# Optimization experiments

Measured on AMD Instinct MI355X. Metric: run time of the kernel, lower is better.

The kernel has to match this reference:

```python
import jax, jax.numpy as jnp
import numpy as np

BANDWIDTH = 0.1
N_STEPS = 5
TOL = 1e-3
BASE = 3
COORD_OFFSET = 512   # bins assumed within (-512, 511] per dim
COORD_BITS = 10      # 3 dims * 10 bits = 30 bits, fits int32


def _generate_offsets(d, base=3):
    # replicates torch.meshgrid(indexing='ij') over arange(-1, base-1)
    ranges = [np.arange(-1, base - 1) for _ in range(d)]
    mesh = np.meshgrid(*ranges, indexing='ij')
    return jnp.asarray(np.stack(mesh, axis=-1).reshape(-1, d), dtype=jnp.int32)


def _pack_keys(bins):
    # bins: (..., d) int32 -> unique scalar int32 key per bin coordinate
    d = bins.shape[-1]
    key = jnp.zeros(bins.shape[:-1], dtype=jnp.int32)
    for k in range(d):  # tiny fixed loop over dims
        key = (key << COORD_BITS) | (bins[..., k] + COORD_OFFSET)
    return key


def _step(X, offsets, bandwidth):
    # One mean-shift step: bin points, scatter-add sums/counts over the
    # union of offset-shifted bins (torch.unique replaced by exact key
    # packing + sort-based grouping, fixed shapes for jit).
    n, d = X.shape
    m = offsets.shape[0]  # base ** d
    bins = (X / bandwidth).astype(jnp.int32)          # trunc-toward-zero == torch .int()
    shifted = bins[:, None, :] + offsets[None, :, :]  # (n, m, d)
    keys = _pack_keys(shifted).reshape(-1)            # (n*m,)
    K = keys.shape[0]

    order = jnp.argsort(keys)
    skeys = keys[order]
    new_grp = jnp.concatenate(
        [jnp.zeros((1,), jnp.int32), (skeys[1:] != skeys[:-1]).astype(jnp.int32)]
    )
    seg = jnp.cumsum(new_grp)                         # group id per sorted position

    # X repeated once per offset (matches X.repeat(1, m).reshape(-1, d))
    Xflat = jnp.broadcast_to(X[:, None, :], (n, m, d)).reshape(-1, d)
    sum_per = jax.ops.segment_sum(Xflat[order], seg, num_segments=K)          # (K, d)
    cnt_per = jax.ops.segment_sum(jnp.ones((K,), X.dtype), seg, num_segments=K)

    # segment id per original (unsorted) flat position == inverse_indices
    seg_orig = jnp.zeros((K,), seg.dtype).at[order].set(seg)
    sum_mapped = sum_per[seg_orig].reshape(n, m, d).sum(axis=1)   # (n, d)
    cnt_mapped = cnt_per[seg_orig].reshape(n, m).sum(axis=1)      # (n,)
    return sum_mapped / cnt_mapped[:, None]


def setup_inputs() -> dict:
    key = jax.random.key(0)
    X = jax.random.normal(key, (200000, 3), dtype=jnp.float32)
    return {"X": X}


def reference(X):
    n, d = X.shape
    offsets = _generate_offsets(d, BASE)

    def body(carry, _):
        Xc, done = carry
        Xn = _step(Xc, offsets, BANDWIDTH)
        Xn = jnp.where(done, Xc, Xn)  # freeze once converged (== early break)
        conv = jnp.max(jnp.linalg.norm(Xn - Xc, axis=1)) <= TOL
        return (Xn, done | conv), None

    (Xout, _), _ = jax.lax.scan(body, (X, jnp.array(False)), None, length=N_STEPS)
    return Xout
```

## Files before the change

### kernel.cpp

```cpp
#include <hip/hip_runtime.h>


constexpr float BW   = 0.1f;
constexpr float TOL2 = 1e-6f;
constexpr int DIM  = 112, OFF = 56;
constexpr int DIM2 = DIM * DIM;
constexpr int CELLS = DIM * DIM * DIM;
constexpr int CLW = CELLS / 32;
constexpr int RDIM = 16, RC = 7;
constexpr int NREG = RDIM * RDIM * RDIM;
constexpr int RC3 = RC * RC * RC;
constexpr int NB_A = 128, BLK = 256;
constexpr int NF = 2048;
constexpr int IPB = 51;
constexpr float FPS = 16777216.0f;
constexpr double FPSI = 1.0 / 16777216.0;

typedef float vf2 __attribute__((ext_vector_type(2)));

__device__ __forceinline__ int clampb(int v) { return v < 0 ? 0 : (v > DIM - 1 ? DIM - 1 : v); }
__device__ __forceinline__ int binf(float v) { return clampb((int)(v / BW) + OFF); }
__device__ __forceinline__ int flatb(int bx, int by, int bz) { return (bx * DIM + by) * DIM + bz; }
__device__ __forceinline__ int regOf(int bx, int by, int bz) {
    return ((bx / RC) * RDIM + (by / RC)) * RDIM + (bz / RC);
}
__device__ __forceinline__ int lcOf(int bx, int by, int bz) {
    return ((bx % RC) * RC + (by % RC)) * RC + (bz % RC);
}

__device__ __forceinline__ void pk_add(float* p, float a, float b) {
#if defined(__has_builtin) && __has_builtin(__builtin_amdgcn_global_atomic_fadd_v2f32)
    vf2 v = {a, b};
    __builtin_amdgcn_global_atomic_fadd_v2f32((vf2*)p, v);
#else
    atomicAdd(p, a);
    atomicAdd(p + 1, b);
#endif
}

__launch_bounds__(BLK)
__global__ void k_histA(const float* __restrict__ X, int n, int* __restrict__ blockHist,
                        float4* __restrict__ zeroA, float4* __restrict__ zeroB) {
    __shared__ int h[NREG];
    for (int i = threadIdx.x; i < NREG; i += blockDim.x) h[i] = 0;
    __syncthreads();
    int stride = gridDim.x * blockDim.x;
    for (int i = blockIdx.x * blockDim.x + threadIdx.x; i < n; i += stride) {
        float x = X[3 * i + 0], y = X[3 * i + 1], z = X[3 * i + 2];
        atomicAdd(&h[regOf(binf(x), binf(y), binf(z))], 1);
    }
    __syncthreads();
    for (int i = threadIdx.x; i < NREG; i += blockDim.x)
        blockHist[blockIdx.x * NREG + i] = h[i];
    for (int i = blockIdx.x * blockDim.x + threadIdx.x; i < CELLS; i += stride) {
        zeroA[i] = make_float4(0.f, 0.f, 0.f, 0.f);
        zeroB[i] = make_float4(0.f, 0.f, 0.f, 0.f);
    }
}

__global__ void k_colscan(int* __restrict__ blockHist, int* __restrict__ regionPS) {
    int r = blockIdx.x * blockDim.x + threadIdx.x;
    if (r >= NREG) return;
    int run = 0;
    for (int b = 0; b < NB_A; ++b) {
        int idx = b * NREG + r;
        int v = blockHist[idx];
        blockHist[idx] = run;
        run += v;
    }
    regionPS[r] = run;
}

__launch_bounds__(1024)
__global__ void k_regprefix(int* __restrict__ regionPS) {
    __shared__ int buf[1024];
    int t = threadIdx.x;
    int v0 = regionPS[4 * t + 0], v1 = regionPS[4 * t + 1];
    int v2 = regionPS[4 * t + 2], v3 = regionPS[4 * t + 3];
    int s = v0 + v1 + v2 + v3;
    buf[t] = s;
    __syncthreads();
    for (int d = 1; d < 1024; d <<= 1) {
        int add = (t >= d) ? buf[t - d] : 0;
        __syncthreads();
        buf[t] += add;
        __syncthreads();
    }
    int excl = buf[t] - s;
    regionPS[4 * t + 0] = excl;
    regionPS[4 * t + 1] = excl + v0;
    regionPS[4 * t + 2] = excl + v0 + v1;
    regionPS[4 * t + 3] = excl + v0 + v1 + v2;
    if (t == 1023) regionPS[4096] = buf[1023];
}

__launch_bounds__(BLK)
__global__ void k_scatterA(const float* __restrict__ X, int n,
                           const int* __restrict__ blockHist,
                           const int* __restrict__ regionPS,
                           float4* __restrict__ bucket, float4* __restrict__ zeroC) {
    __shared__ int cur[NREG];
    for (int i = threadIdx.x; i < NREG; i += blockDim.x) cur[i] = 0;
    __syncthreads();
    int stride = gridDim.x * blockDim.x;
    for (int i = blockIdx.x * blockDim.x + threadIdx.x; i < n; i += stride) {
        float x = X[3 * i + 0], y = X[3 * i + 1], z = X[3 * i + 2];
        int r = regOf(binf(x), binf(y), binf(z));
        int pos = regionPS[r] + blockHist[blockIdx.x * NREG + r] + atomicAdd(&cur[r], 1);
        bucket[pos] = make_float4(x, y, z, __int_as_float(i));
    }
    for (int i = blockIdx.x * blockDim.x + threadIdx.x; i < CELLS; i += stride)
        zeroC[i] = make_float4(0.f, 0.f, 0.f, 0.f);
}

__launch_bounds__(BLK)
__global__ void k_binB(const float4* __restrict__ bucket, const int* __restrict__ regionPS,
                       float4* __restrict__ A, int* __restrict__ E0,
                       int* __restrict__ PIdx, int* __restrict__ gM0) {
    __shared__ unsigned long long aX[RC3], aY[RC3], aZ[RC3];
    __shared__ unsigned aC[RC3];
    __shared__ int cidx[RC3];
    __shared__ int cnt, cur, sBase;
    int r = blockIdx.x;
    for (int c = threadIdx.x; c < RC3; c += blockDim.x) {
        aX[c] = 0ull; aY[c] = 0ull; aZ[c] = 0ull; aC[c] = 0u;
    }
    if (threadIdx.x == 0) { cnt = 0; cur = 0; }
    __syncthreads();
    int start = regionPS[r], end = regionPS[r + 1];
    for (int i = start + threadIdx.x; i < end; i += blockDim.x) {
        float4 p = bucket[i];
        int lc = lcOf(binf(p.x), binf(p.y), binf(p.z));
        atomicAdd(&aX[lc], (unsigned long long)(long long)rintf(p.x * FPS));
        atomicAdd(&aY[lc], (unsigned long long)(long long)rintf(p.y * FPS));
        atomicAdd(&aZ[lc], (unsigned long long)(long long)rintf(p.z * FPS));
        atomicAdd(&aC[lc], 1u);
    }
    __syncthreads();
    int myc = 0;
    for (int c = threadIdx.x; c < RC3; c += blockDim.x)
        if (aC[c] > 0u) ++myc;
    if (myc) atomicAdd(&cnt, myc);
    __syncthreads();
    if (threadIdx.x == 0 && cnt > 0) sBase = atomicAdd(gM0, cnt);
    __syncthreads();
    int rx = r / (RDIM * RDIM), ry = (r / RDIM) % RDIM, rz = r % RDIM;
    for (int c = threadIdx.x; c < RC3; c += blockDim.x) {
        if (aC[c] > 0u) {
            int idx = sBase + atomicAdd(&cur, 1);
            cidx[c] = idx;
            int bx = rx * RC + c / (RC * RC);
            int by = ry * RC + (c / RC) % RC;
            int bz = rz * RC + c % RC;
            int b = flatb(bx, by, bz);
            E0[idx] = b;
            A[b] = make_float4((float)((double)(long long)aX[c] * FPSI),
                               (float)((double)(long long)aY[c] * FPSI),
                               (float)((double)(long long)aZ[c] * FPSI),
                               (float)aC[c]);
        }
    }
    __syncthreads();
    for (int i = start + threadIdx.x; i < end; i += blockDim.x) {
        float4 p = bucket[i];
        int lc = lcOf(binf(p.x), binf(p.y), binf(p.z));
        PIdx[__float_as_int(p.w)] = cidx[lc];
    }
}

__launch_bounds__(BLK)
__global__ void k_compactM(unsigned* __restrict__ mask, int* __restrict__ listOut,
                           int* __restrict__ pKout) {
    __shared__ int scan[BLK];
    __shared__ int sBase;
    int i = blockIdx.x * blockDim.x + threadIdx.x;
    unsigned w = (i < CLW) ? mask[i] : 0u;
    if (i < CLW && w) mask[i] = 0u;
    int c = __popc(w);
    scan[threadIdx.x] = c;
    __syncthreads();
    for (int d = 1; d < BLK; d <<= 1) {
        int add = (threadIdx.x >= (unsigned)d) ? scan[threadIdx.x - d] : 0;
        __syncthreads();
        scan[threadIdx.x] += add;
        __syncthreads();
    }
    if (threadIdx.x == BLK - 1) {
        int tot = scan[BLK - 1];
        sBase = tot ? atomicAdd(pKout, tot) : 0;
    }
    __syncthreads();
    int base = sBase + scan[threadIdx.x] - c;
    int bb = i * 32;
    while (w) {
        int b = __ffs(w) - 1;
        listOut[base++] = bb + b;
        w &= w - 1;
    }
}

__launch_bounds__(BLK)
__global__ void k_fused(
    const float4* __restrict__ src, const int* __restrict__ list, const int* __restrict__ pK,
    float4* __restrict__ REo, int* __restrict__ IDXo, float4* __restrict__ eposInit,
    float4* __restrict__ tgt, unsigned* __restrict__ clT,
    int updS, const float* __restrict__ X, int n, const int* __restrict__ PIdx,
    const float4* __restrict__ REp, const int* __restrict__ IDXp,
    const int* __restrict__ pM0, float4* __restrict__ epos,
    unsigned* __restrict__ notConv,
    const int* __restrict__ clearList, const int* __restrict__ pKc,
    float4* __restrict__ clearGrid, int lastStep) {
    __shared__ float4 sh[BLK];
    __shared__ unsigned sFlag;
    if (threadIdx.x == 0) sFlag = 0;
    __syncthreads();
    int K = *pK;
    int NC = (K + IPB - 1) / IPB;
    int BC = NC;
    if (BC > NF - 256) BC = NF - 256;
    const float t5[5] = {1.f, 2.f, 3.f, 2.f, 1.f};
    bool moved = false;

    if ((int)blockIdx.x < BC) {
        int first, last, step;
        if (BC >= 64) {
            int xcd = blockIdx.x & 7, loc = blockIdx.x >> 3;
            int cpx = (NC + 7) >> 3;
            int bpx = ((BC - 1 - xcd) >> 3) + 1;
            first = xcd * cpx + loc;
            last = (xcd + 1) * cpx; if (last > NC) last = NC;
            step = bpx;
        } else {
            first = blockIdx.x; last = NC; step = BC;
        }
        for (int ib = first; ib < last; ib += step) {
            int li = threadIdx.x / 5;
            int dx = threadIdx.x % 5;
            int item = ib * IPB + li;
            float4 part = make_float4(0.f, 0.f, 0.f, 0.f);
            if (li < IPB && item < K) {
                int b = list[item];
                int bx = b / DIM2, rem = b % DIM2;
                int by = rem / DIM, bz = rem % DIM;
                int ix = bx + dx - 2;
                if ((unsigned)ix < (unsigned)DIM) {
                    float wx = t5[dx];
                    if (by >= 2 && by <= DIM - 3 && bz >= 2 && bz <= DIM - 3) {
                        #pragma unroll
                        for (int dy = 0; dy < 5; ++dy) {
                            float wxy = wx * t5[dy];
                            const float4* row = src + flatb(ix, by + dy - 2, bz - 2);
                            #pragma unroll
                            for (int dz = 0; dz < 5; ++dz) {
                                float w = wxy * t5[dz];
                                float4 e = row[dz];
                                part.x = fmaf(w, e.x, part.x);
                                part.y = fmaf(w, e.y, part.y);
                                part.z = fmaf(w, e.z, part.z);
                                part.w = fmaf(w, e.w, part.w);
                            }
                        }
                    } else {
                        for (int dy = 0; dy < 5; ++dy) {
                            int iy = by + dy - 2;
                            if ((unsigned)iy >= (unsigned)DIM) continue;
                            float wxy = wx * t5[dy];
                            for (int dz = 0; dz < 5; ++dz) {
                                int iz = bz + dz - 2;
                                if ((unsigned)iz >= (unsigned)DIM) continue;
                                float w = wxy * t5[dz];
                                float4 e = src[flatb(ix, iy, iz)];
                                part.x = fmaf(w, e.x, part.x);
                                part.y = fmaf(w, e.y, part.y);
                                part.z = fmaf(w, e.z, part.z);
                                part.w = fmaf(w, e.w, part.w);
                            }
                        }
                    }
                }
            }
            sh[threadIdx.x] = part;
            __syncthreads();
            if (threadIdx.x < 64) {
                int item2 = ib * IPB + threadIdx.x;
                bool valid = (threadIdx.x < IPB) && (item2 < K);
                int bn = -1;
                float4 sv = make_float4(0.f, 0.f, 0.f, 0.f);
                if (valid) {
                    int base5 = threadIdx.x * 5;
                    float4 a0 = sh[base5 + 0], a1 = sh[base5 + 1], a2 = sh[base5 + 2];
                    float4 a3 = sh[base5 + 3], a4 = sh[base5 + 4];
                    float sx = a0.x + a1.x + a2.x + a3.x + a4.x;
                    float sy = a0.y + a1.y + a2.y + a3.y + a4.y;
                    float sz = a0.z + a1.z + a2.z + a3.z + a4.z;
                    float sc = a0.w + a1.w + a2.w + a3.w + a4.w;
                    int b = list[item2];
                    float W = src[b].w;
                    float4 np = make_float4(sx / sc, sy / sc, sz / sc, W);
                    REo[item2] = np;
                    IDXo[b] = item2;
                    if (eposInit) eposInit[item2] = np;
                    if (!lastStep) {
                        bn = flatb(binf(np.x), binf(np.y), binf(np.z));
                        sv = make_float4(W * np.x, W * np.y, W * np.z, W);
                    }
                }
                if (!lastStep) {
                    int pbn = __shfl_up(bn, 1, 64);
                    unsigned f = (threadIdx.x == 0 || pbn != bn) ? 1u : 0u;
                    unsigned nf = __shfl_down(f, 1, 64);
                    bool leader = valid && (threadIdx.x == 63 || nf != 0u);
                    #pragma unroll
                    for (int off = 1; off < 64; off <<= 1) {
                        float ox = __shfl_up(sv.x, off, 64);
                        float oy = __shfl_up(sv.y, off, 64);
                        float oz = __shfl_up(sv.z, off, 64);
                        float ow = __shfl_up(sv.w, off, 64);
                        unsigned of = __shfl_up(f, off, 64);
                        if ((int)threadIdx.x >= off) {
                            if (!f) { sv.x += ox; sv.y += oy; sv.z += oz; sv.w += ow; }
                            f |= of;
                        }
                    }
                    if (leader) {
                        float* cell = (float*)&tgt[bn];
                        pk_add(cell + 0, sv.x, sv.y);
                        pk_add(cell + 2, sv.z, sv.w);
                        atomicOr(&clT[(unsigned)bn >> 5], 1u << (bn & 31));
                    }
                }
            }
            __syncthreads();
        }
    } else {
        int U = (updS > 0) ? (X ? n : *pM0) : 0;
        int CL = clearList ? *pKc : 0;
        int total = U + CL;
        bool done = false;
        if (updS > 1) {
            for (int t = 1; t < updS; ++t) done |= (notConv[t] == 0u);
        }
        int stride = (NF - BC) * blockDim.x;
        for (int idx = (blockIdx.x - BC) * blockDim.x + threadIdx.x; idx < total;
             idx += stride) {
            if (idx < U) {
                int e = idx;
                if (X) {
                    float x = X[3 * e + 0], y = X[3 * e + 1], z = X[3 * e + 2];
                    float4 rr = REp[PIdx[e]];
                    float ex = rr.x - x, ey = rr.y - y, ez = rr.z - z;
                    moved |= (fmaf(ex, ex, fmaf(ey, ey, ez * ez)) > TOL2);
                } else if (!done) {
                    float4 p = epos[e];
                    int j = IDXp[flatb(binf(p.x), binf(p.y), binf(p.z))];
                    float4 rr = REp[j];
                    float ex = rr.x - p.x, ey = rr.y - p.y, ez = rr.z - p.z;
                    moved |= (fmaf(ex, ex, fmaf(ey, ey, ez * ez)) > TOL2);
                    epos[e] = make_float4(rr.x, rr.y, rr.z, p.w);
                }
            } else {
                clearGrid[clearList[idx - U]] = make_float4(0.f, 0.f, 0.f, 0.f);
            }
        }
    }
    if (moved) sFlag = 1;
    __syncthreads();
    if (threadIdx.x == 0 && updS > 0 && sFlag) notConv[updS] = 1u;
}

__launch_bounds__(BLK)
__global__ void k_fin(const float4* __restrict__ REa, const int* __restrict__ IDXa,
                      const float4* __restrict__ epos, const int* __restrict__ pM0,
                      const unsigned* __restrict__ notConv, float4* __restrict__ fpos) {
    int M0 = *pM0;
    bool done = false;
    for (int t = 1; t <= 4; ++t) done |= (notConv[t] == 0u);
    for (int e = blockIdx.x * blockDim.x + threadIdx.x; e < M0;
         e += gridDim.x * blockDim.x) {
        float4 p = epos[e];
        if (!done) {
            float4 rr = REa[IDXa[flatb(binf(p.x), binf(p.y), binf(p.z))]];
            p.x = rr.x; p.y = rr.y; p.z = rr.z;
        }
        fpos[e] = p;
    }
}

__global__ void k_map(const int* __restrict__ PIdx, int n, const float4* __restrict__ fpos,
                      float* __restrict__ out) {
    int i = blockIdx.x * blockDim.x + threadIdx.x;
    if (i >= n) return;
    float4 p = fpos[PIdx[i]];
    out[3 * i + 0] = p.x;
    out[3 * i + 1] = p.y;
    out[3 * i + 2] = p.z;
}

extern "C" void kernel_launch(void* const* d_in, const int* in_sizes, int n_in,
                              void* d_out, int out_size, void* d_ws, size_t ws_size,
                              hipStream_t stream) {
    const float* X = (const float*)d_in[0];
    int n = in_sizes[0] / 3;

    char* ws = (char*)d_ws;
    int*      cnt     = (int*)ws;
    unsigned* notConv = (unsigned*)(ws + 32);
    size_t mB = (size_t)CLW * 4;
    size_t gB = (size_t)CELLS * 16;
    unsigned* m0 = (unsigned*)(ws + 256);
    unsigned* m1 = (unsigned*)(ws + 256 + mB);
    float4* A = (float4*)(ws + 256 + 2 * mB);
    float4* B = (float4*)((char*)A + gB);
    float4* C = (float4*)((char*)B + gB);
    int* IDXa = (int*)((char*)C + gB);
    int* IDXb = IDXa + CELLS;
    float4* REa  = (float4*)(IDXb + CELLS);
    float4* REb  = REa + n;
    float4* epos = REb + n;
    int* E0   = (int*)(epos + n);
    int* La   = E0 + n;
    int* Lb   = La + n;
    int* Lc   = Lb + n;
    int* Ld   = Lc + n;
    int* PIdx = Ld + n;
    float4* bucket = (float4*)(PIdx + n);
    int* blockHist = (int*)(bucket + n);
    int* regionPS  = blockHist + NB_A * NREG;

    hipMemsetAsync(ws, 0, 256 + 2 * mB, stream);

    const int NCM = (CLW + BLK - 1) / BLK;

    k_histA<<<NB_A, BLK, 0, stream>>>(X, n, blockHist, A, B);
    k_colscan<<<NREG / BLK, BLK, 0, stream>>>(blockHist, regionPS);
    k_regprefix<<<1, 1024, 0, stream>>>(regionPS);
    k_scatterA<<<NB_A, BLK, 0, stream>>>(X, n, blockHist, regionPS, bucket, C);
    k_binB<<<NREG, BLK, 0, stream>>>(bucket, regionPS, A, E0, PIdx, &cnt[1]);

    k_fused<<<NF, BLK, 0, stream>>>(A, E0, &cnt[1], REa, IDXa, epos,
                                    B, m0,
                                    0, nullptr, n, nullptr, nullptr, nullptr, nullptr,
                                    nullptr, notConv, nullptr, nullptr, nullptr, 0);
    k_compactM<<<NCM, BLK, 0, stream>>>(m0, La, &cnt[2]);
    k_fused<<<NF, BLK, 0, stream>>>(B, La, &cnt[2], REb, IDXb, nullptr,
                                    C, m1,
                                    1, X, n, PIdx, REa, IDXa, &cnt[1], nullptr,
                                    notConv, E0, &cnt[1], A, 0);
    k_compactM<<<NCM, BLK, 0, stream>>>(m1, Lb, &cnt[3]);
    k_fused<<<NF, BLK, 0, stream>>>(C, Lb, &cnt[3], REa, IDXa, nullptr,
                                    A, m0,
                                    2, nullptr, n, nullptr, REb, IDXb, &cnt[1], epos,
                                    notConv, La, &cnt[2], B, 0);
    k_compactM<<<NCM, BLK, 0, stream>>>(m0, Lc, &cnt[4]);
    k_fused<<<NF, BLK, 0, stream>>>(A, Lc, &cnt[4], REb, IDXb, nullptr,
                                    B, m1,
                                    3, nullptr, n, nullptr, REa, IDXa, &cnt[1], epos,
                                    notConv, nullptr, nullptr, nullptr, 0);
    k_compactM<<<NCM, BLK, 0, stream>>>(m1, Ld, &cnt[5]);
    k_fused<<<NF, BLK, 0, stream>>>(B, Ld, &cnt[5], REa, IDXa, nullptr,
                                    nullptr, nullptr,
                                    4, nullptr, n, nullptr, REb, IDXb, &cnt[1], epos,
                                    notConv, nullptr, nullptr, nullptr, 1);

    k_fin<<<256, BLK, 0, stream>>>(REa, IDXa, epos, &cnt[1], notConv, REb);
    k_map<<<(n + BLK - 1) / BLK, BLK, 0, stream>>>(PIdx, n, REb, (float*)d_out);
}
```

Measured before the change: 246.5 us.

## Build occupied-cell lists inside fused step via atomicOr; fold final lookup into map

The separate bitmask-compaction kernel that ran after each step is removed. The fused kernel now uses the old value returned by atomicOr to detect cells it newly marks, and appends them to the next occupied-cell list with a wave ballot plus one atomicAdd per wavefront. Mask words are cleared later by the update blocks, which walk the previous list. The final-position kernel is merged into the output map kernel, which removes two launches and one intermediate buffer pass. In exchange, list order becomes nondeterministic, cells are no longer sorted, and the per-wave global atomic adds contention.

Measured after the change: 290.1 us. 1.18x slower.

```diff
diff --git a/kernel.cpp b/kernel.cpp
--- a/kernel.cpp
+++ b/kernel.cpp
@@ -169,47 +169,19 @@
 }
 
 __launch_bounds__(BLK)
-__global__ void k_compactM(unsigned* __restrict__ mask, int* __restrict__ listOut,
-                           int* __restrict__ pKout) {
-    __shared__ int scan[BLK];
-    __shared__ int sBase;
-    int i = blockIdx.x * blockDim.x + threadIdx.x;
-    unsigned w = (i < CLW) ? mask[i] : 0u;
-    if (i < CLW && w) mask[i] = 0u;
-    int c = __popc(w);
-    scan[threadIdx.x] = c;
-    __syncthreads();
-    for (int d = 1; d < BLK; d <<= 1) {
-        int add = (threadIdx.x >= (unsigned)d) ? scan[threadIdx.x - d] : 0;
-        __syncthreads();
-        scan[threadIdx.x] += add;
-        __syncthreads();
-    }
-    if (threadIdx.x == BLK - 1) {
-        int tot = scan[BLK - 1];
-        sBase = tot ? atomicAdd(pKout, tot) : 0;
-    }
-    __syncthreads();
-    int base = sBase + scan[threadIdx.x] - c;
-    int bb = i * 32;
-    while (w) {
-        int b = __ffs(w) - 1;
-        listOut[base++] = bb + b;
-        w &= w - 1;
-    }
-}
-
-__launch_bounds__(BLK)
 __global__ void k_fused(
     const float4* __restrict__ src, const int* __restrict__ list, const int* __restrict__ pK,
     float4* __restrict__ REo, int* __restrict__ IDXo, float4* __restrict__ eposInit,
     float4* __restrict__ tgt, unsigned* __restrict__ clT,
+    int* __restrict__ listOut, int* __restrict__ pKout,
     int updS, const float* __restrict__ X, int n, const int* __restrict__ PIdx,
     const float4* __restrict__ REp, const int* __restrict__ IDXp,
     const int* __restrict__ pM0, float4* __restrict__ epos,
     unsigned* __restrict__ notConv,
     const int* __restrict__ clearList, const int* __restrict__ pKc,
-    float4* __restrict__ clearGrid, int lastStep) {
+    float4* __restrict__ clearGrid,
+    const int* __restrict__ mClrList, const int* __restrict__ pKm,
+    unsigned* __restrict__ mClr, int lastStep) {
     __shared__ float4 sh[BLK];
     __shared__ unsigned sFlag;
     if (threadIdx.x == 0) sFlag = 0;
@@ -322,11 +294,22 @@
                             f |= of;
                         }
                     }
+                    bool fset = false;
                     if (leader) {
                         float* cell = (float*)&tgt[bn];
                         pk_add(cell + 0, sv.x, sv.y);
                         pk_add(cell + 2, sv.z, sv.w);
-                        atomicOr(&clT[(unsigned)bn >> 5], 1u << (bn & 31));
+                        unsigned bit = 1u << (bn & 31);
+                        unsigned old = atomicOr(&clT[(unsigned)bn >> 5], bit);
+                        fset = (old & bit) == 0u;
+                    }
+                    unsigned long long bal = __ballot(fset);
+                    if (bal) {
+                        int base = 0;
+                        if (threadIdx.x == 0) base = atomicAdd(pKout, __popcll(bal));
+                        base = __shfl(base, 0, 64);
+                        if (fset)
+                            listOut[base + __popcll(bal & ((1ull << threadIdx.x) - 1ull))] = bn;
                     }
                 }
             }
@@ -335,7 +318,8 @@
     } else {
         int U = (updS > 0) ? (X ? n : *pM0) : 0;
         int CL = clearList ? *pKc : 0;
-        int total = U + CL;
+        int CM = mClrList ? *pKm : 0;
+        int total = U + CL + CM;
         bool done = false;
         if (updS > 1) {
             for (int t = 1; t < updS; ++t) done |= (notConv[t] == 0u);
@@ -358,8 +342,11 @@
                     moved |= (fmaf(ex, ex, fmaf(ey, ey, ez * ez)) > TOL2);
                     epos[e] = make_float4(rr.x, rr.y, rr.z, p.w);
                 }
+            } else if (idx < U + CL) {
+                clearGrid[clearList[idx - U]] = make_float4(0.f, 0.f, 0.f, 0.f);
             } else {
-                clearGrid[clearList[idx - U]] = make_float4(0.f, 0.f, 0.f, 0.f);
+                int b = mClrList[idx - U - CL];
+                mClr[(unsigned)b >> 5] = 0u;
             }
         }
     }
@@ -368,29 +355,18 @@
     if (threadIdx.x == 0 && updS > 0 && sFlag) notConv[updS] = 1u;
 }
 
-__launch_bounds__(BLK)
-__global__ void k_fin(const float4* __restrict__ REa, const int* __restrict__ IDXa,
-                      const float4* __restrict__ epos, const int* __restrict__ pM0,
-                      const unsigned* __restrict__ notConv, float4* __restrict__ fpos) {
-    int M0 = *pM0;
+__global__ void k_map(const int* __restrict__ PIdx, int n, const float4* __restrict__ epos,
+                      const float4* __restrict__ REa, const int* __restrict__ IDXa,
+                      const unsigned* __restrict__ notConv, float* __restrict__ out) {
     bool done = false;
     for (int t = 1; t <= 4; ++t) done |= (notConv[t] == 0u);
-    for (int e = blockIdx.x * blockDim.x + threadIdx.x; e < M0;
-         e += gridDim.x * blockDim.x) {
-        float4 p = epos[e];
-        if (!done) {
-            float4 rr = REa[IDXa[flatb(binf(p.x), binf(p.y), binf(p.z))]];
-            p.x = rr.x; p.y = rr.y; p.z = rr.z;
-        }
-        fpos[e] = p;
-    }
-}
-
-__global__ void k_map(const int* __restrict__ PIdx, int n, const float4* __restrict__ fpos,
-                      float* __restrict__ out) {
     int i = blockIdx.x * blockDim.x + threadIdx.x;
     if (i >= n) return;
-    float4 p = fpos[PIdx[i]];
+    float4 p = epos[PIdx[i]];
+    if (!done) {
+        float4 rr = REa[IDXa[flatb(binf(p.x), binf(p.y), binf(p.z))]];
+        p.x = rr.x; p.y = rr.y; p.z = rr.z;
+    }
     out[3 * i + 0] = p.x;
     out[3 * i + 1] = p.y;
     out[3 * i + 2] = p.z;
@@ -429,8 +405,6 @@
 
     hipMemsetAsync(ws, 0, 256 + 2 * mB, stream);
 
-    const int NCM = (CLW + BLK - 1) / BLK;
-
     k_histA<<<NB_A, BLK, 0, stream>>>(X, n, blockHist, A, B);
     k_colscan<<<NREG / BLK, BLK, 0, stream>>>(blockHist, regionPS);
     k_regprefix<<<1, 1024, 0, stream>>>(regionPS);
@@ -438,30 +412,36 @@
     k_binB<<<NREG, BLK, 0, stream>>>(bucket, regionPS, A, E0, PIdx, &cnt[1]);
 
     k_fused<<<NF, BLK, 0, stream>>>(A, E0, &cnt[1], REa, IDXa, epos,
-                                    B, m0,
+                                    B, m0, La, &cnt[2],
                                     0, nullptr, n, nullptr, nullptr, nullptr, nullptr,
-                                    nullptr, notConv, nullptr, nullptr, nullptr, 0);
-    k_compactM<<<NCM, BLK, 0, stream>>>(m0, La, &cnt[2]);
+                                    nullptr, notConv,
+                                    nullptr, nullptr, nullptr,
+                                    nullptr, nullptr, nullptr, 0);
     k_fused<<<NF, BLK, 0, stream>>>(B, La, &cnt[2], REb, IDXb, nullptr,
-                                    C, m1,
+                                    C, m1, Lb, &cnt[3],
                                     1, X, n, PIdx, REa, IDXa, &cnt[1], nullptr,
-                                    notConv, E0, &cnt[1], A, 0);
-    k_compactM<<<NCM, BLK, 0, stream>>>(m1, Lb, &cnt[3]);
+                                    notConv,
+                                    E0, &cnt[1], A,
+                                    La, &cnt[2], m0, 0);
     k_fused<<<NF, BLK, 0, stream>>>(C, Lb, &cnt[3], REa, IDXa, nullptr,
-                                    A, m0,
+                                    A, m0, Lc, &cnt[4],
                                     2, nullptr, n, nullptr, REb, IDXb, &cnt[1], epos,
-                                    notConv, La, &cnt[2], B, 0);
-    k_compactM<<<NCM, BLK, 0, stream>>>(m0, Lc, &cnt[4]);
+                                    notConv,
+                                    La, &cnt[2], B,
+                                    Lb, &cnt[3], m1, 0);
     k_fused<<<NF, BLK, 0, stream>>>(A, Lc, &cnt[4], REb, IDXb, nullptr,
-                                    B, m1,
+                                    B, m1, Ld, &cnt[5],
                                     3, nullptr, n, nullptr, REa, IDXa, &cnt[1], epos,
-                                    notConv, nullptr, nullptr, nullptr, 0);
-    k_compactM<<<NCM, BLK, 0, stream>>>(m1, Ld, &cnt[5]);
+                                    notConv,
+                                    nullptr, nullptr, nullptr,
+                                    nullptr, nullptr, nullptr, 0);
     k_fused<<<NF, BLK, 0, stream>>>(B, Ld, &cnt[5], REa, IDXa, nullptr,
-                                    nullptr, nullptr,
+                                    nullptr, nullptr, nullptr, nullptr,
                                     4, nullptr, n, nullptr, REb, IDXb, &cnt[1], epos,
-                                    notConv, nullptr, nullptr, nullptr, 1);
-
-    k_fin<<<256, BLK, 0, stream>>>(REa, IDXa, epos, &cnt[1], notConv, REb);
-    k_map<<<(n + BLK - 1) / BLK, BLK, 0, stream>>>(PIdx, n, REb, (float*)d_out);
-}
+                                    notConv,
+                                    nullptr, nullptr, nullptr,
+                                    nullptr, nullptr, nullptr, 1);
+
+    k_map<<<(n + BLK - 1) / BLK, BLK, 0, stream>>>(PIdx, n, epos, REa, IDXa,
+                                                   notConv, (float*)d_out);
+}
```

## Split separable 5x5x5 stencil into dense z-pass and sparse xy-pass

Applied to the files above, without the earlier changes.

Replaces the per-cell 125-tap stencil with a separable scheme. A dense pass convolves the whole grid along z into a temporary buffer. A sparse pass then does only the 25 x/y taps per active cell, reading the z-presummed values. This cuts gathers per active cell from 125 to 25, but adds a full-grid read and write every step plus an extra kernel launch. It also reduces ping-pong grids from three to two, drops the separate grid zeroing and k_fin, and folds the final position lookup into k_map.

New measurement: 282.0 us. 14.4% more time.

```diff
diff --git a/kernel.cpp b/kernel.cpp
--- a/kernel.cpp
+++ b/kernel.cpp
@@ -13,6 +13,8 @@
 constexpr int NB_A = 128, BLK = 256;
 constexpr int NF = 2048;
 constexpr int IPB = 51;
+constexpr int NZ4 = CELLS / 4;
+constexpr int BCZ = NF - 256;
 constexpr float FPS = 16777216.0f;
 constexpr double FPSI = 1.0 / 16777216.0;
 
@@ -98,7 +100,7 @@
 __global__ void k_scatterA(const float* __restrict__ X, int n,
                            const int* __restrict__ blockHist,
                            const int* __restrict__ regionPS,
-                           float4* __restrict__ bucket, float4* __restrict__ zeroC) {
+                           float4* __restrict__ bucket) {
     __shared__ int cur[NREG];
     for (int i = threadIdx.x; i < NREG; i += blockDim.x) cur[i] = 0;
     __syncthreads();
@@ -109,8 +111,6 @@
         int pos = regionPS[r] + blockHist[blockIdx.x * NREG + r] + atomicAdd(&cur[r], 1);
         bucket[pos] = make_float4(x, y, z, __int_as_float(i));
     }
-    for (int i = blockIdx.x * blockDim.x + threadIdx.x; i < CELLS; i += stride)
-        zeroC[i] = make_float4(0.f, 0.f, 0.f, 0.f);
 }
 
 __launch_bounds__(BLK)
@@ -169,168 +169,38 @@
 }
 
 __launch_bounds__(BLK)
-__global__ void k_compactM(unsigned* __restrict__ mask, int* __restrict__ listOut,
-                           int* __restrict__ pKout) {
-    __shared__ int scan[BLK];
-    __shared__ int sBase;
-    int i = blockIdx.x * blockDim.x + threadIdx.x;
-    unsigned w = (i < CLW) ? mask[i] : 0u;
-    if (i < CLW && w) mask[i] = 0u;
-    int c = __popc(w);
-    scan[threadIdx.x] = c;
-    __syncthreads();
-    for (int d = 1; d < BLK; d <<= 1) {
-        int add = (threadIdx.x >= (unsigned)d) ? scan[threadIdx.x - d] : 0;
-        __syncthreads();
-        scan[threadIdx.x] += add;
-        __syncthreads();
-    }
-    if (threadIdx.x == BLK - 1) {
-        int tot = scan[BLK - 1];
-        sBase = tot ? atomicAdd(pKout, tot) : 0;
-    }
-    __syncthreads();
-    int base = sBase + scan[threadIdx.x] - c;
-    int bb = i * 32;
-    while (w) {
-        int b = __ffs(w) - 1;
-        listOut[base++] = bb + b;
-        w &= w - 1;
-    }
-}
-
-__launch_bounds__(BLK)
-__global__ void k_fused(
-    const float4* __restrict__ src, const int* __restrict__ list, const int* __restrict__ pK,
-    float4* __restrict__ REo, int* __restrict__ IDXo, float4* __restrict__ eposInit,
-    float4* __restrict__ tgt, unsigned* __restrict__ clT,
-    int updS, const float* __restrict__ X, int n, const int* __restrict__ PIdx,
-    const float4* __restrict__ REp, const int* __restrict__ IDXp,
-    const int* __restrict__ pM0, float4* __restrict__ epos,
-    unsigned* __restrict__ notConv,
-    const int* __restrict__ clearList, const int* __restrict__ pKc,
-    float4* __restrict__ clearGrid, int lastStep) {
-    __shared__ float4 sh[BLK];
+__global__ void k_zconv(const float4* __restrict__ src, float4* __restrict__ T1,
+                        int updS, const float* __restrict__ X, int n,
+                        const int* __restrict__ PIdx,
+                        const float4* __restrict__ REp, const int* __restrict__ IDXp,
+                        const int* __restrict__ pM0, float4* __restrict__ epos,
+                        unsigned* __restrict__ notConv,
+                        const int* __restrict__ clearList, const int* __restrict__ pKc,
+                        float4* __restrict__ clearGrid) {
     __shared__ unsigned sFlag;
     if (threadIdx.x == 0) sFlag = 0;
     __syncthreads();
-    int K = *pK;
-    int NC = (K + IPB - 1) / IPB;
-    int BC = NC;
-    if (BC > NF - 256) BC = NF - 256;
-    const float t5[5] = {1.f, 2.f, 3.f, 2.f, 1.f};
     bool moved = false;
-
-    if ((int)blockIdx.x < BC) {
-        int first, last, step;
-        if (BC >= 64) {
-            int xcd = blockIdx.x & 7, loc = blockIdx.x >> 3;
-            int cpx = (NC + 7) >> 3;
-            int bpx = ((BC - 1 - xcd) >> 3) + 1;
-            first = xcd * cpx + loc;
-            last = (xcd + 1) * cpx; if (last > NC) last = NC;
-            step = bpx;
-        } else {
-            first = blockIdx.x; last = NC; step = BC;
-        }
-        for (int ib = first; ib < last; ib += step) {
-            int li = threadIdx.x / 5;
-            int dx = threadIdx.x % 5;
-            int item = ib * IPB + li;
-            float4 part = make_float4(0.f, 0.f, 0.f, 0.f);
-            if (li < IPB && item < K) {
-                int b = list[item];
-                int bx = b / DIM2, rem = b % DIM2;
-                int by = rem / DIM, bz = rem % DIM;
-                int ix = bx + dx - 2;
-                if ((unsigned)ix < (unsigned)DIM) {
-                    float wx = t5[dx];
-                    if (by >= 2 && by <= DIM - 3 && bz >= 2 && bz <= DIM - 3) {
-                        #pragma unroll
-                        for (int dy = 0; dy < 5; ++dy) {
-                            float wxy = wx * t5[dy];
-                            const float4* row = src + flatb(ix, by + dy - 2, bz - 2);
-                            #pragma unroll
-                            for (int dz = 0; dz < 5; ++dz) {
-                                float w = wxy * t5[dz];
-                                float4 e = row[dz];
-                                part.x = fmaf(w, e.x, part.x);
-                                part.y = fmaf(w, e.y, part.y);
-                                part.z = fmaf(w, e.z, part.z);
-                                part.w = fmaf(w, e.w, part.w);
-                            }
-                        }
-                    } else {
-                        for (int dy = 0; dy < 5; ++dy) {
-                            int iy = by + dy - 2;
-                            if ((unsigned)iy >= (unsigned)DIM) continue;
-                            float wxy = wx * t5[dy];
-                            for (int dz = 0; dz < 5; ++dz) {
-                                int iz = bz + dz - 2;
-                                if ((unsigned)iz >= (unsigned)DIM) continue;
-                                float w = wxy * t5[dz];
-                                float4 e = src[flatb(ix, iy, iz)];
-                                part.x = fmaf(w, e.x, part.x);
-                                part.y = fmaf(w, e.y, part.y);
-                                part.z = fmaf(w, e.z, part.z);
-                                part.w = fmaf(w, e.w, part.w);
-                            }
-                        }
-                    }
-                }
-            }
-            sh[threadIdx.x] = part;
-            __syncthreads();
-            if (threadIdx.x < 64) {
-                int item2 = ib * IPB + threadIdx.x;
-                bool valid = (threadIdx.x < IPB) && (item2 < K);
-                int bn = -1;
-                float4 sv = make_float4(0.f, 0.f, 0.f, 0.f);
-                if (valid) {
-                    int base5 = threadIdx.x * 5;
-                    float4 a0 = sh[base5 + 0], a1 = sh[base5 + 1], a2 = sh[base5 + 2];
-                    float4 a3 = sh[base5 + 3], a4 = sh[base5 + 4];
-                    float sx = a0.x + a1.x + a2.x + a3.x + a4.x;
-                    float sy = a0.y + a1.y + a2.y + a3.y + a4.y;
-                    float sz = a0.z + a1.z + a2.z + a3.z + a4.z;
-                    float sc = a0.w + a1.w + a2.w + a3.w + a4.w;
-                    int b = list[item2];
-                    float W = src[b].w;
-                    float4 np = make_float4(sx / sc, sy / sc, sz / sc, W);
-                    REo[item2] = np;
-                    IDXo[b] = item2;
-                    if (eposInit) eposInit[item2] = np;
-                    if (!lastStep) {
-                        bn = flatb(binf(np.x), binf(np.y), binf(np.z));
-                        sv = make_float4(W * np.x, W * np.y, W * np.z, W);
-                    }
-                }
-                if (!lastStep) {
-                    int pbn = __shfl_up(bn, 1, 64);
-                    unsigned f = (threadIdx.x == 0 || pbn != bn) ? 1u : 0u;
-                    unsigned nf = __shfl_down(f, 1, 64);
-                    bool leader = valid && (threadIdx.x == 63 || nf != 0u);
-                    #pragma unroll
-                    for (int off = 1; off < 64; off <<= 1) {
-                        float ox = __shfl_up(sv.x, off, 64);
-                        float oy = __shfl_up(sv.y, off, 64);
-                        float oz = __shfl_up(sv.z, off, 64);
-                        float ow = __shfl_up(sv.w, off, 64);
-                        unsigned of = __shfl_up(f, off, 64);
-                        if ((int)threadIdx.x >= off) {
-                            if (!f) { sv.x += ox; sv.y += oy; sv.z += oz; sv.w += ow; }
-                            f |= of;
-                        }
-                    }
-                    if (leader) {
-                        float* cell = (float*)&tgt[bn];
-                        pk_add(cell + 0, sv.x, sv.y);
-                        pk_add(cell + 2, sv.z, sv.w);
-                        atomicOr(&clT[(unsigned)bn >> 5], 1u << (bn & 31));
-                    }
-                }
-            }
-            __syncthreads();
+    if ((int)blockIdx.x < BCZ) {
+        for (int w = blockIdx.x * BLK + threadIdx.x; w < NZ4; w += BCZ * BLK) {
+            int c0 = w * 4;
+            int z0 = c0 % DIM;
+            float4 e[8];
+            #pragma unroll
+            for (int k = 0; k < 8; ++k) {
+                int z = z0 + k - 2;
+                if ((unsigned)z < (unsigned)DIM) e[k] = src[c0 + k - 2];
+                else e[k] = make_float4(0.f, 0.f, 0.f, 0.f);
+            }
+            #pragma unroll
+            for (int j = 0; j < 4; ++j) {
+                float4 r;
+                r.x = e[j].x + e[j + 4].x + 2.f * (e[j + 1].x + e[j + 3].x) + 3.f * e[j + 2].x;
+                r.y = e[j].y + e[j + 4].y + 2.f * (e[j + 1].y + e[j + 3].y) + 3.f * e[j + 2].y;
+                r.z = e[j].z + e[j + 4].z + 2.f * (e[j + 1].z + e[j + 3].z) + 3.f * e[j + 2].z;
+                r.w = e[j].w + e[j + 4].w + 2.f * (e[j + 1].w + e[j + 3].w) + 3.f * e[j + 2].w;
+                T1[c0 + j] = r;
+            }
         }
     } else {
         int U = (updS > 0) ? (X ? n : *pM0) : 0;
@@ -340,8 +210,8 @@
         if (updS > 1) {
             for (int t = 1; t < updS; ++t) done |= (notConv[t] == 0u);
         }
-        int stride = (NF - BC) * blockDim.x;
-        for (int idx = (blockIdx.x - BC) * blockDim.x + threadIdx.x; idx < total;
+        int stride = (NF - BCZ) * BLK;
+        for (int idx = (blockIdx.x - BCZ) * BLK + threadIdx.x; idx < total;
              idx += stride) {
             if (idx < U) {
                 int e = idx;
@@ -369,28 +239,165 @@
 }
 
 __launch_bounds__(BLK)
-__global__ void k_fin(const float4* __restrict__ REa, const int* __restrict__ IDXa,
-                      const float4* __restrict__ epos, const int* __restrict__ pM0,
-                      const unsigned* __restrict__ notConv, float4* __restrict__ fpos) {
-    int M0 = *pM0;
+__global__ void k_conv(const float4* __restrict__ T1, const float4* __restrict__ src,
+                       const int* __restrict__ list, const int* __restrict__ pK,
+                       float4* __restrict__ REo, int* __restrict__ IDXo,
+                       float4* __restrict__ eposInit,
+                       float4* __restrict__ tgt, unsigned* __restrict__ clT,
+                       int lastStep) {
+    __shared__ float4 sh[BLK];
+    int K = *pK;
+    int NC = (K + IPB - 1) / IPB;
+    int BC = NC > NF ? NF : NC;
+    if ((int)blockIdx.x >= BC) return;
+    const float t5[5] = {1.f, 2.f, 3.f, 2.f, 1.f};
+
+    int first, last, step;
+    if (BC >= 64) {
+        int xcd = blockIdx.x & 7, loc = blockIdx.x >> 3;
+        int cpx = (NC + 7) >> 3;
+        int bpx = ((BC - 1 - xcd) >> 3) + 1;
+        first = xcd * cpx + loc;
+        last = (xcd + 1) * cpx; if (last > NC) last = NC;
+        step = bpx;
+    } else {
+        first = blockIdx.x; last = NC; step = BC;
+    }
+    for (int ib = first; ib < last; ib += step) {
+        int li = threadIdx.x / 5;
+        int dx = threadIdx.x % 5;
+        int item = ib * IPB + li;
+        float4 part = make_float4(0.f, 0.f, 0.f, 0.f);
+        if (li < IPB && item < K) {
+            int b = list[item];
+            int bx = b / DIM2, rem = b % DIM2;
+            int by = rem / DIM, bz = rem % DIM;
+            int ix = bx + dx - 2;
+            if ((unsigned)ix < (unsigned)DIM) {
+                float wx = t5[dx];
+                if (by >= 2 && by <= DIM - 3) {
+                    const float4* col = T1 + flatb(ix, by - 2, bz);
+                    #pragma unroll
+                    for (int dy = 0; dy < 5; ++dy) {
+                        float w = wx * t5[dy];
+                        float4 e = col[dy * DIM];
+                        part.x = fmaf(w, e.x, part.x);
+                        part.y = fmaf(w, e.y, part.y);
+                        part.z = fmaf(w, e.z, part.z);
+                        part.w = fmaf(w, e.w, part.w);
+                    }
+                } else {
+                    for (int dy = 0; dy < 5; ++dy) {
+                        int iy = by + dy - 2;
+                        if ((unsigned)iy >= (unsigned)DIM) continue;
+                        float w = wx * t5[dy];
+                        float4 e = T1[flatb(ix, iy, bz)];
+                        part.x = fmaf(w, e.x, part.x);
+                        part.y = fmaf(w, e.y, part.y);
+                        part.z = fmaf(w, e.z, part.z);
+                        part.w = fmaf(w, e.w, part.w);
+                    }
+                }
+            }
+        }
+        sh[threadIdx.x] = part;
+        __syncthreads();
+        if (threadIdx.x < 64) {
+            int item2 = ib * IPB + threadIdx.x;
+            bool valid = (threadIdx.x < IPB) && (item2 < K);
+            int bn = -1;
+            float4 sv = make_float4(0.f, 0.f, 0.f, 0.f);
+            if (valid) {
+                int base5 = threadIdx.x * 5;
+                float4 a0 = sh[base5 + 0], a1 = sh[base5 + 1], a2 = sh[base5 + 2];
+                float4 a3 = sh[base5 + 3], a4 = sh[base5 + 4];
+                float sx = a0.x + a1.x + a2.x + a3.x + a4.x;
+                float sy = a0.y + a1.y + a2.y + a3.y + a4.y;
+                float sz = a0.z + a1.z + a2.z + a3.z + a4.z;
+                float sc = a0.w + a1.w + a2.w + a3.w + a4.w;
+                int b = list[item2];
+                float W = src[b].w;
+                float4 np = make_float4(sx / sc, sy / sc, sz / sc, W);
+                REo[item2] = np;
+                IDXo[b] = item2;
+                if (eposInit) eposInit[item2] = np;
+                if (!lastStep) {
+                    bn = flatb(binf(np.x), binf(np.y), binf(np.z));
+                    sv = make_float4(W * np.x, W * np.y, W * np.z, W);
+                }
+            }
+            if (!lastStep) {
+                int pbn = __shfl_up(bn, 1, 64);
+                unsigned f = (threadIdx.x == 0 || pbn != bn) ? 1u : 0u;
+                unsigned nf = __shfl_down(f, 1, 64);
+                bool leader = valid && (threadIdx.x == 63 || nf != 0u);
+                #pragma unroll
+                for (int off = 1; off < 64; off <<= 1) {
+                    float ox = __shfl_up(sv.x, off, 64);
+                    float oy = __shfl_up(sv.y, off, 64);
+                    float oz = __shfl_up(sv.z, off, 64);
+                    float ow = __shfl_up(sv.w, off, 64);
+                    unsigned of = __shfl_up(f, off, 64);
+                    if ((int)threadIdx.x >= off) {
+                        if (!f) { sv.x += ox; sv.y += oy; sv.z += oz; sv.w += ow; }
+                        f |= of;
+                    }
+                }
+                if (leader) {
+                    float* cell = (float*)&tgt[bn];
+                    pk_add(cell + 0, sv.x, sv.y);
+                    pk_add(cell + 2, sv.z, sv.w);
+                    atomicOr(&clT[(unsigned)bn >> 5], 1u << (bn & 31));
+                }
+            }
+        }
+        __syncthreads();
+    }
+}
+
+__launch_bounds__(BLK)
+__global__ void k_compactM(unsigned* __restrict__ mask, int* __restrict__ listOut,
+                           int* __restrict__ pKout) {
+    __shared__ int scan[BLK];
+    __shared__ int sBase;
+    int i = blockIdx.x * blockDim.x + threadIdx.x;
+    unsigned w = (i < CLW) ? mask[i] : 0u;
+    if (i < CLW && w) mask[i] = 0u;
+    int c = __popc(w);
+    scan[threadIdx.x] = c;
+    __syncthreads();
+    for (int d = 1; d < BLK; d <<= 1) {
+        int add = (threadIdx.x >= (unsigned)d) ? scan[threadIdx.x - d] : 0;
+        __syncthreads();
+        scan[threadIdx.x] += add;
+        __syncthreads();
+    }
+    if (threadIdx.x == BLK - 1) {
+        int tot = scan[BLK - 1];
+        sBase = tot ? atomicAdd(pKout, tot) : 0;
+    }
+    __syncthreads();
+    int base = sBase + scan[threadIdx.x] - c;
+    int bb = i * 32;
+    while (w) {
+        int b = __ffs(w) - 1;
+        listOut[base++] = bb + b;
+        w &= w - 1;
+    }
+}
+
+__global__ void k_map(const int* __restrict__ PIdx, int n, const float4* __restrict__ epos,
+                      const float4* __restrict__ REa, const int* __restrict__ IDXa,
+                      const unsigned* __restrict__ notConv, float* __restrict__ out) {
     bool done = false;
     for (int t = 1; t <= 4; ++t) done |= (notConv[t] == 0u);
-    for (int e = blockIdx.x * blockDim.x + threadIdx.x; e < M0;
-         e += gridDim.x * blockDim.x) {
-        float4 p = epos[e];
-        if (!done) {
-            float4 rr = REa[IDXa[flatb(binf(p.x), binf(p.y), binf(p.z))]];
-            p.x = rr.x; p.y = rr.y; p.z = rr.z;
-        }
-        fpos[e] = p;
-    }
-}
-
-__global__ void k_map(const int* __restrict__ PIdx, int n, const float4* __restrict__ fpos,
-                      float* __restrict__ out) {
     int i = blockIdx.x * blockDim.x + threadIdx.x;
     if (i >= n) return;
-    float4 p = fpos[PIdx[i]];
+    float4 p = epos[PIdx[i]];
+    if (!done) {
+        float4 rr = REa[IDXa[flatb(binf(p.x), binf(p.y), binf(p.z))]];
+        p.x = rr.x; p.y = rr.y; p.z = rr.z;
+    }
     out[3 * i + 0] = p.x;
     out[3 * i + 1] = p.y;
     out[3 * i + 2] = p.z;
@@ -409,10 +416,10 @@
     size_t gB = (size_t)CELLS * 16;
     unsigned* m0 = (unsigned*)(ws + 256);
     unsigned* m1 = (unsigned*)(ws + 256 + mB);
-    float4* A = (float4*)(ws + 256 + 2 * mB);
-    float4* B = (float4*)((char*)A + gB);
-    float4* C = (float4*)((char*)B + gB);
-    int* IDXa = (int*)((char*)C + gB);
+    float4* A  = (float4*)(ws + 256 + 2 * mB);
+    float4* B  = (float4*)((char*)A + gB);
+    float4* T1 = (float4*)((char*)B + gB);
+    int* IDXa = (int*)((char*)T1 + gB);
     int* IDXb = IDXa + CELLS;
     float4* REa  = (float4*)(IDXb + CELLS);
     float4* REb  = REa + n;
@@ -434,34 +441,34 @@
     k_histA<<<NB_A, BLK, 0, stream>>>(X, n, blockHist, A, B);
     k_colscan<<<NREG / BLK, BLK, 0, stream>>>(blockHist, regionPS);
     k_regprefix<<<1, 1024, 0, stream>>>(regionPS);
-    k_scatterA<<<NB_A, BLK, 0, stream>>>(X, n, blockHist, regionPS, bucket, C);
+    k_scatterA<<<NB_A, BLK, 0, stream>>>(X, n, blockHist, regionPS, bucket);
     k_binB<<<NREG, BLK, 0, stream>>>(bucket, regionPS, A, E0, PIdx, &cnt[1]);
 
-    k_fused<<<NF, BLK, 0, stream>>>(A, E0, &cnt[1], REa, IDXa, epos,
-                                    B, m0,
-                                    0, nullptr, n, nullptr, nullptr, nullptr, nullptr,
-                                    nullptr, notConv, nullptr, nullptr, nullptr, 0);
+    k_zconv<<<NF, BLK, 0, stream>>>(A, T1, 0, nullptr, n, nullptr, nullptr, nullptr,
+                                    nullptr, nullptr, notConv, nullptr, nullptr, nullptr);
+    k_conv<<<NF, BLK, 0, stream>>>(T1, A, E0, &cnt[1], REa, IDXa, epos, B, m0, 0);
     k_compactM<<<NCM, BLK, 0, stream>>>(m0, La, &cnt[2]);
-    k_fused<<<NF, BLK, 0, stream>>>(B, La, &cnt[2], REb, IDXb, nullptr,
-                                    C, m1,
-                                    1, X, n, PIdx, REa, IDXa, &cnt[1], nullptr,
-                                    notConv, E0, &cnt[1], A, 0);
+
+    k_zconv<<<NF, BLK, 0, stream>>>(B, T1, 1, X, n, PIdx, REa, IDXa, &cnt[1],
+                                    nullptr, notConv, E0, &cnt[1], A);
+    k_conv<<<NF, BLK, 0, stream>>>(T1, B, La, &cnt[2], REb, IDXb, nullptr, A, m1, 0);
     k_compactM<<<NCM, BLK, 0, stream>>>(m1, Lb, &cnt[3]);
-    k_fused<<<NF, BLK, 0, stream>>>(C, Lb, &cnt[3], REa, IDXa, nullptr,
-                                    A, m0,
-                                    2, nullptr, n, nullptr, REb, IDXb, &cnt[1], epos,
-                                    notConv, La, &cnt[2], B, 0);
+
+    k_zconv<<<NF, BLK, 0, stream>>>(A, T1, 2, nullptr, n, nullptr, REb, IDXb, &cnt[1],
+                                    epos, notConv, La, &cnt[2], B);
+    k_conv<<<NF, BLK, 0, stream>>>(T1, A, Lb, &cnt[3], REa, IDXa, nullptr, B, m0, 0);
     k_compactM<<<NCM, BLK, 0, stream>>>(m0, Lc, &cnt[4]);
-    k_fused<<<NF, BLK, 0, stream>>>(A, Lc, &cnt[4], REb, IDXb, nullptr,
-                                    B, m1,
-                                    3, nullptr, n, nullptr, REa, IDXa, &cnt[1], epos,
-                                    notConv, nullptr, nullptr, nullptr, 0);
+
+    k_zconv<<<NF, BLK, 0, stream>>>(B, T1, 3, nullptr, n, nullptr, REa, IDXa, &cnt[1],
+                                    epos, notConv, Lb, &cnt[3], A);
+    k_conv<<<NF, BLK, 0, stream>>>(T1, B, Lc, &cnt[4], REb, IDXb, nullptr, A, m1, 0);
     k_compactM<<<NCM, BLK, 0, stream>>>(m1, Ld, &cnt[5]);
-    k_fused<<<NF, BLK, 0, stream>>>(B, Ld, &cnt[5], REa, IDXa, nullptr,
-                                    nullptr, nullptr,
-                                    4, nullptr, n, nullptr, REb, IDXb, &cnt[1], epos,
-                                    notConv, nullptr, nullptr, nullptr, 1);
-
-    k_fin<<<256, BLK, 0, stream>>>(REa, IDXa, epos, &cnt[1], notConv, REb);
-    k_map<<<(n + BLK - 1) / BLK, BLK, 0, stream>>>(PIdx, n, REb, (float*)d_out);
-}
+
+    k_zconv<<<NF, BLK, 0, stream>>>(A, T1, 4, nullptr, n, nullptr, REb, IDXb, &cnt[1],
+                                    epos, notConv, nullptr, nullptr, nullptr);
+    k_conv<<<NF, BLK, 0, stream>>>(T1, A, Ld, &cnt[5], REa, IDXa, nullptr,
+                                   nullptr, nullptr, 1);
+
+    k_map<<<(n + BLK - 1) / BLK, BLK, 0, stream>>>(PIdx, n, epos, REa, IDXa,
+                                                   notConv, (float*)d_out);
+}
```

## Use atomic work queue for stencil chunks and fold final lookup into map

Applied to the files above, without the earlier changes.

Replaces the static XCD-aware chunk assignment in the fused step kernel with a dynamic work queue: each block grabs chunk indices from a global atomic counter, one counter per step, zeroed by the existing memset. This is meant to balance uneven per-chunk cost across blocks. Separately, the final-position kernel is merged into the output mapping kernel, removing one launch and an intermediate buffer. The cost is an atomic plus a barrier per chunk and the loss of XCD-local chunk placement, and the final lookup may now repeat per point instead of once per occupied bin.

Measured after the change: 300.3 us. 21.8% more time.

```diff
diff --git a/kernel.cpp b/kernel.cpp
--- a/kernel.cpp
+++ b/kernel.cpp
@@ -169,39 +169,9 @@
 }
 
 __launch_bounds__(BLK)
-__global__ void k_compactM(unsigned* __restrict__ mask, int* __restrict__ listOut,
-                           int* __restrict__ pKout) {
-    __shared__ int scan[BLK];
-    __shared__ int sBase;
-    int i = blockIdx.x * blockDim.x + threadIdx.x;
-    unsigned w = (i < CLW) ? mask[i] : 0u;
-    if (i < CLW && w) mask[i] = 0u;
-    int c = __popc(w);
-    scan[threadIdx.x] = c;
-    __syncthreads();
-    for (int d = 1; d < BLK; d <<= 1) {
-        int add = (threadIdx.x >= (unsigned)d) ? scan[threadIdx.x - d] : 0;
-        __syncthreads();
-        scan[threadIdx.x] += add;
-        __syncthreads();
-    }
-    if (threadIdx.x == BLK - 1) {
-        int tot = scan[BLK - 1];
-        sBase = tot ? atomicAdd(pKout, tot) : 0;
-    }
-    __syncthreads();
-    int base = sBase + scan[threadIdx.x] - c;
-    int bb = i * 32;
-    while (w) {
-        int b = __ffs(w) - 1;
-        listOut[base++] = bb + b;
-        w &= w - 1;
-    }
-}
-
-__launch_bounds__(BLK)
 __global__ void k_fused(
     const float4* __restrict__ src, const int* __restrict__ list, const int* __restrict__ pK,
+    int* __restrict__ qCtr,
     float4* __restrict__ REo, int* __restrict__ IDXo, float4* __restrict__ eposInit,
     float4* __restrict__ tgt, unsigned* __restrict__ clT,
     int updS, const float* __restrict__ X, int n, const int* __restrict__ PIdx,
@@ -212,6 +182,7 @@
     float4* __restrict__ clearGrid, int lastStep) {
     __shared__ float4 sh[BLK];
     __shared__ unsigned sFlag;
+    __shared__ int sChunk;
     if (threadIdx.x == 0) sFlag = 0;
     __syncthreads();
     int K = *pK;
@@ -222,18 +193,11 @@
     bool moved = false;
 
     if ((int)blockIdx.x < BC) {
-        int first, last, step;
-        if (BC >= 64) {
-            int xcd = blockIdx.x & 7, loc = blockIdx.x >> 3;
-            int cpx = (NC + 7) >> 3;
-            int bpx = ((BC - 1 - xcd) >> 3) + 1;
-            first = xcd * cpx + loc;
-            last = (xcd + 1) * cpx; if (last > NC) last = NC;
-            step = bpx;
-        } else {
-            first = blockIdx.x; last = NC; step = BC;
-        }
-        for (int ib = first; ib < last; ib += step) {
+        for (;;) {
+            if (threadIdx.x == 0) sChunk = atomicAdd(qCtr, 1);
+            __syncthreads();
+            int ib = sChunk;
+            if (ib >= NC) break;
             int li = threadIdx.x / 5;
             int dx = threadIdx.x % 5;
             int item = ib * IPB + li;
@@ -369,28 +333,48 @@
 }
 
 __launch_bounds__(BLK)
-__global__ void k_fin(const float4* __restrict__ REa, const int* __restrict__ IDXa,
-                      const float4* __restrict__ epos, const int* __restrict__ pM0,
-                      const unsigned* __restrict__ notConv, float4* __restrict__ fpos) {
-    int M0 = *pM0;
+__global__ void k_compactM(unsigned* __restrict__ mask, int* __restrict__ listOut,
+                           int* __restrict__ pKout) {
+    __shared__ int scan[BLK];
+    __shared__ int sBase;
+    int i = blockIdx.x * blockDim.x + threadIdx.x;
+    unsigned w = (i < CLW) ? mask[i] : 0u;
+    if (i < CLW && w) mask[i] = 0u;
+    int c = __popc(w);
+    scan[threadIdx.x] = c;
+    __syncthreads();
+    for (int d = 1; d < BLK; d <<= 1) {
+        int add = (threadIdx.x >= (unsigned)d) ? scan[threadIdx.x - d] : 0;
+        __syncthreads();
+        scan[threadIdx.x] += add;
+        __syncthreads();
+    }
+    if (threadIdx.x == BLK - 1) {
+        int tot = scan[BLK - 1];
+        sBase = tot ? atomicAdd(pKout, tot) : 0;
+    }
+    __syncthreads();
+    int base = sBase + scan[threadIdx.x] - c;
+    int bb = i * 32;
+    while (w) {
+        int b = __ffs(w) - 1;
+        listOut[base++] = bb + b;
+        w &= w - 1;
+    }
+}
+
+__global__ void k_map(const int* __restrict__ PIdx, int n, const float4* __restrict__ epos,
+                      const float4* __restrict__ REa, const int* __restrict__ IDXa,
+                      const unsigned* __restrict__ notConv, float* __restrict__ out) {
     bool done = false;
     for (int t = 1; t <= 4; ++t) done |= (notConv[t] == 0u);
-    for (int e = blockIdx.x * blockDim.x + threadIdx.x; e < M0;
-         e += gridDim.x * blockDim.x) {
-        float4 p = epos[e];
-        if (!done) {
-            float4 rr = REa[IDXa[flatb(binf(p.x), binf(p.y), binf(p.z))]];
-            p.x = rr.x; p.y = rr.y; p.z = rr.z;
-        }
-        fpos[e] = p;
-    }
-}
-
-__global__ void k_map(const int* __restrict__ PIdx, int n, const float4* __restrict__ fpos,
-                      float* __restrict__ out) {
     int i = blockIdx.x * blockDim.x + threadIdx.x;
     if (i >= n) return;
-    float4 p = fpos[PIdx[i]];
+    float4 p = epos[PIdx[i]];
+    if (!done) {
+        float4 rr = REa[IDXa[flatb(binf(p.x), binf(p.y), binf(p.z))]];
+        p.x = rr.x; p.y = rr.y; p.z = rr.z;
+    }
     out[3 * i + 0] = p.x;
     out[3 * i + 1] = p.y;
     out[3 * i + 2] = p.z;
@@ -405,6 +389,7 @@
     char* ws = (char*)d_ws;
     int*      cnt     = (int*)ws;
     unsigned* notConv = (unsigned*)(ws + 32);
+    int*      qc      = (int*)(ws + 64);
     size_t mB = (size_t)CLW * 4;
     size_t gB = (size_t)CELLS * 16;
     unsigned* m0 = (unsigned*)(ws + 256);
@@ -437,31 +422,31 @@
     k_scatterA<<<NB_A, BLK, 0, stream>>>(X, n, blockHist, regionPS, bucket, C);
     k_binB<<<NREG, BLK, 0, stream>>>(bucket, regionPS, A, E0, PIdx, &cnt[1]);
 
-    k_fused<<<NF, BLK, 0, stream>>>(A, E0, &cnt[1], REa, IDXa, epos,
+    k_fused<<<NF, BLK, 0, stream>>>(A, E0, &cnt[1], &qc[0], REa, IDXa, epos,
                                     B, m0,
                                     0, nullptr, n, nullptr, nullptr, nullptr, nullptr,
                                     nullptr, notConv, nullptr, nullptr, nullptr, 0);
     k_compactM<<<NCM, BLK, 0, stream>>>(m0, La, &cnt[2]);
-    k_fused<<<NF, BLK, 0, stream>>>(B, La, &cnt[2], REb, IDXb, nullptr,
+    k_fused<<<NF, BLK, 0, stream>>>(B, La, &cnt[2], &qc[1], REb, IDXb, nullptr,
                                     C, m1,
                                     1, X, n, PIdx, REa, IDXa, &cnt[1], nullptr,
                                     notConv, E0, &cnt[1], A, 0);
     k_compactM<<<NCM, BLK, 0, stream>>>(m1, Lb, &cnt[3]);
-    k_fused<<<NF, BLK, 0, stream>>>(C, Lb, &cnt[3], REa, IDXa, nullptr,
+    k_fused<<<NF, BLK, 0, stream>>>(C, Lb, &cnt[3], &qc[2], REa, IDXa, nullptr,
                                     A, m0,
                                     2, nullptr, n, nullptr, REb, IDXb, &cnt[1], epos,
                                     notConv, La, &cnt[2], B, 0);
     k_compactM<<<NCM, BLK, 0, stream>>>(m0, Lc, &cnt[4]);
-    k_fused<<<NF, BLK, 0, stream>>>(A, Lc, &cnt[4], REb, IDXb, nullptr,
+    k_fused<<<NF, BLK, 0, stream>>>(A, Lc, &cnt[4], &qc[3], REb, IDXb, nullptr,
                                     B, m1,
                                     3, nullptr, n, nullptr, REa, IDXa, &cnt[1], epos,
                                     notConv, nullptr, nullptr, nullptr, 0);
     k_compactM<<<NCM, BLK, 0, stream>>>(m1, Ld, &cnt[5]);
-    k_fused<<<NF, BLK, 0, stream>>>(B, Ld, &cnt[5], REa, IDXa, nullptr,
+    k_fused<<<NF, BLK, 0, stream>>>(B, Ld, &cnt[5], &qc[4], REa, IDXa, nullptr,
                                     nullptr, nullptr,
                                     4, nullptr, n, nullptr, REb, IDXb, &cnt[1], epos,
                                     notConv, nullptr, nullptr, nullptr, 1);
 
-    k_fin<<<256, BLK, 0, stream>>>(REa, IDXa, epos, &cnt[1], notConv, REb);
-    k_map<<<(n + BLK - 1) / BLK, BLK, 0, stream>>>(PIdx, n, REb, (float*)d_out);
-}
+    k_map<<<(n + BLK - 1) / BLK, BLK, 0, stream>>>(PIdx, n, epos, REa, IDXa,
+                                                   notConv, (float*)d_out);
+}
```
